# Performance work log

Measured on AMD Instinct MI355X. Metric: run time of the kernel, lower is better.

Reference implementation:

```python
import jax, jax.numpy as jnp
import numpy as np

N = 50000      # nodes
E = 800000     # edges (before self loops)
D_IN = 256     # input feature dim
H = 64         # hidden dim
HEADS = 4
NEG_SLOPE = 0.2  # PyG GATConv default


def setup_inputs() -> dict:
    key = jax.random.key(0)
    ks = jax.random.split(key, 24)

    def w(k, shape, fan_in):
        return jax.random.normal(k, shape, jnp.float32) / np.sqrt(fan_in)

    inp = {
        "x": jax.random.normal(ks[0], (N, D_IN), jnp.float32),
        "edge_index": jax.random.randint(ks[1], (2, E), 0, N, jnp.int64),
        # GCN layers
        "W0": w(ks[2], (D_IN, H), D_IN), "b0": jnp.zeros((H,), jnp.float32),
        "W1": w(ks[3], (H, H), H),       "b1": jnp.zeros((H,), jnp.float32),
        "W2": w(ks[4], (H, H), H),       "b2": jnp.zeros((H,), jnp.float32),
        # GAT
        "Wg": w(ks[5], (H, HEADS * H), H),
        "att_src": w(ks[6], (HEADS, H), H),
        "att_dst": w(ks[7], (HEADS, H), H),
        "bg": jnp.zeros((H,), jnp.float32),
        # classifier MLP: H -> H//2 -> 2
        "Wc1": w(ks[8], (H, H // 2), H),   "bc1": jnp.zeros((H // 2,), jnp.float32),
        "Wc2": w(ks[9], (H // 2, 2), H // 2), "bc2": jnp.zeros((2,), jnp.float32),
        # reconstructor MLP: H -> H -> D_IN
        "Wr1": w(ks[10], (H, H), H),       "br1": jnp.zeros((H,), jnp.float32),
        "Wr2": w(ks[11], (H, D_IN), H),    "br2": jnp.zeros((D_IN,), jnp.float32),
    }
    return inp


def reference(x, edge_index, W0, b0, W1, b1, W2, b2,
              Wg, att_src, att_dst, bg,
              Wc1, bc1, Wc2, bc2, Wr1, br1, Wr2, br2):
    # add self loops (PyG default for both GCNConv and GATConv)
    loops = jnp.arange(N, dtype=edge_index.dtype)
    src = jnp.concatenate([edge_index[0], loops])  # [E+N]
    dst = jnp.concatenate([edge_index[1], loops])

    # symmetric GCN normalization: deg^-1/2[src] * deg^-1/2[dst]
    deg = jax.ops.segment_sum(jnp.ones_like(src, jnp.float32), dst, num_segments=N)
    dinv = jnp.where(deg > 0, jax.lax.rsqrt(deg), 0.0)
    norm = dinv[src] * dinv[dst]  # [E+N]

    def gcn(h, W, b):
        msg = (h @ W)[src] * norm[:, None]          # gather + scale
        return jax.ops.segment_sum(msg, dst, num_segments=N) + b

    # stacked GCN with residuals (dropout inactive in eval)
    h = jax.nn.relu(gcn(x, W0, b0))                 # [N, H]
    h = h + jax.nn.relu(gcn(h, W1, b1))
    h = h + jax.nn.relu(gcn(h, W2, b2))

    # GAT layer, 4 heads, concat=False -> mean over heads
    xg = (h @ Wg).reshape(N, HEADS, H)              # [N, heads, H]
    a_s = jnp.einsum('nhf,hf->nh', xg, att_src)     # [N, heads]
    a_d = jnp.einsum('nhf,hf->nh', xg, att_dst)
    e = jax.nn.leaky_relu(a_s[src] + a_d[dst], NEG_SLOPE)  # [E+N, heads]
    m = jax.ops.segment_max(e, dst, num_segments=N)        # segment softmax
    ex = jnp.exp(e - m[dst])
    s = jax.ops.segment_sum(ex, dst, num_segments=N)
    alpha = ex / s[dst]                                     # [E+N, heads]
    hg = jax.ops.segment_sum(xg[src] * alpha[:, :, None], dst, num_segments=N)
    hg = hg.mean(axis=1) + bg                                # [N, H]

    # global mean pool (batch is None)
    h_global = hg.mean(axis=0, keepdims=True)                # [1, H]
    cls = jax.nn.relu(h_global @ Wc1 + bc1) @ Wc2 + bc2      # [1, 2]
    rec = jax.nn.relu(hg @ Wr1 + br1) @ Wr2 + br2            # [N, D_IN]
    return cls, rec, hg
```

## Files before the change

kernel.cpp:

```cpp
#include <hip/hip_runtime.h>

#define DIN 256
#define HD 64
#define NHEAD 4

static inline int cdiv(long a, long b) { return (int)((a + b - 1) / b); }

typedef __attribute__((ext_vector_type(8))) short bf16x8;
typedef __attribute__((ext_vector_type(4))) float f32x4;

__global__ __launch_bounds__(256) void k_filli(int* __restrict__ p, int v, int n) {
  int i = blockIdx.x * 256 + threadIdx.x;
  if (i < n) p[i] = v;
}

__global__ __launch_bounds__(256) void k_count(const int* __restrict__ dst,
                                               int* __restrict__ cnt, int E) {
  int i = blockIdx.x * 256 + threadIdx.x;
  if (i < E) atomicAdd(&cnt[dst[i]], 1);
}

__global__ __launch_bounds__(256) void k_bsum(const int* __restrict__ cnt,
                                              int* __restrict__ bsum, int n) {
  __shared__ int sd[256];
  int i = blockIdx.x * 256 + threadIdx.x;
  sd[threadIdx.x] = (i < n) ? cnt[i] : 0;
  __syncthreads();
  for (int o = 128; o > 0; o >>= 1) {
    if (threadIdx.x < o) sd[threadIdx.x] += sd[threadIdx.x + o];
    __syncthreads();
  }
  if (threadIdx.x == 0) bsum[blockIdx.x] = sd[0];
}

__global__ __launch_bounds__(256) void k_bscan(const int* __restrict__ bsum,
                                               int* __restrict__ boff, int B) {
  __shared__ int sd[256];
  int t = threadIdx.x;
  int v = (t < B) ? bsum[t] : 0;
  sd[t] = v;
  __syncthreads();
  for (int o = 1; o < 256; o <<= 1) {
    int x = (t >= o) ? sd[t - o] : 0;
    __syncthreads();
    sd[t] += x;
    __syncthreads();
  }
  if (t < B) boff[t] = sd[t] - v;
}

__global__ __launch_bounds__(256) void k_rowptr(const int* __restrict__ cnt,
                                                const int* __restrict__ boff,
                                                int* __restrict__ row_ptr,
                                                int* __restrict__ cursor,
                                                float* __restrict__ dinv,
                                                float* __restrict__ gsum, int n, int total) {
  __shared__ int sd[256];
  int t = threadIdx.x;
  int i = blockIdx.x * 256 + t;
  int v = (i < n) ? cnt[i] : 0;
  sd[t] = v;
  __syncthreads();
  for (int o = 1; o < 256; o <<= 1) {
    int x = (t >= o) ? sd[t - o] : 0;
    __syncthreads();
    sd[t] += x;
    __syncthreads();
  }
  if (i < n) {
    int rp = boff[blockIdx.x] + sd[t] - v;
    row_ptr[i] = rp;
    cursor[i] = rp;
    dinv[i] = rsqrtf((float)v);
  }
  if (i == n - 1) row_ptr[n] = total;
  if (blockIdx.x == 0 && t < 64) gsum[t] = 0.f;
}

__global__ __launch_bounds__(256) void k_csrfill(const int* __restrict__ src,
                                                 const int* __restrict__ dst,
                                                 int* __restrict__ cursor,
                                                 int* __restrict__ csr_src, int E, int n) {
  int e = blockIdx.x * 256 + threadIdx.x;
  if (e < E) {
    int pos = atomicAdd(&cursor[dst[e]], 1);
    csr_src[pos] = src[e];
  } else if (e < E + n) {
    int i = e - E;
    int pos = atomicAdd(&cursor[i], 1);
    csr_src[pos] = i;
  }
}

__device__ __forceinline__ unsigned short f2bf(float f) {
  unsigned u = __float_as_uint(f);
  u += 0x7FFFu + ((u >> 16) & 1u);
  return (unsigned short)(u >> 16);
}
__device__ __forceinline__ float bflo(unsigned u) { return __uint_as_float(u << 16); }
__device__ __forceinline__ float bfhi(unsigned u) { return __uint_as_float(u & 0xFFFF0000u); }

template <int KIN, int KOUT, int ATT>
__global__ __launch_bounds__(256, 4) void k_gmfma(const float* __restrict__ A,
                                                  const float* __restrict__ W,
                                                  unsigned short* __restrict__ c16, int n,
                                                  const float* __restrict__ attS,
                                                  const float* __restrict__ attD,
                                                  float* __restrict__ a_s,
                                                  float* __restrict__ a_d) {
  __shared__ unsigned short As[64][64];
  __shared__ unsigned short Wt[64][64];
  const int tid = threadIdx.x;
  const int m0 = blockIdx.x * 64;
  const int n0 = blockIdx.y * 64;
  const int lane = tid & 63;
  const int wid = tid >> 6;
  const int wm = wid * 16;
  const int fr = lane & 15;
  const int fg = lane >> 4;
  f32x4 acc[4] = {{0.f, 0.f, 0.f, 0.f},
                  {0.f, 0.f, 0.f, 0.f},
                  {0.f, 0.f, 0.f, 0.f},
                  {0.f, 0.f, 0.f, 0.f}};

  for (int k0 = 0; k0 < KIN; k0 += 64) {
    {
      int row = tid >> 3;
      int g = tid & 7;
#pragma unroll
      for (int q = 0; q < 2; ++q, row += 32) {
        int gr = m0 + row;
        gr = gr < n ? gr : n - 1;
        const float* ap = A + (size_t)gr * KIN + k0 + g * 8;
        float4 f0 = *(const float4*)ap;
        float4 f1 = *(const float4*)(ap + 4);
        uint4 pk;
        pk.x = (unsigned)f2bf(f0.x) | ((unsigned)f2bf(f0.y) << 16);
        pk.y = (unsigned)f2bf(f0.z) | ((unsigned)f2bf(f0.w) << 16);
        pk.z = (unsigned)f2bf(f1.x) | ((unsigned)f2bf(f1.y) << 16);
        pk.w = (unsigned)f2bf(f1.z) | ((unsigned)f2bf(f1.w) << 16);
        *(uint4*)&As[row][(g ^ (row & 7)) * 8] = pk;
      }
    }
    {
      int col = tid & 63;
      int kb = (tid >> 6) * 16;
      unsigned pk[8];
#pragma unroll
      for (int i = 0; i < 8; ++i) {
        float lo = W[(size_t)(k0 + kb + 2 * i) * KOUT + n0 + col];
        float hi = W[(size_t)(k0 + kb + 2 * i + 1) * KOUT + n0 + col];
        pk[i] = (unsigned)f2bf(lo) | ((unsigned)f2bf(hi) << 16);
      }
      int g0 = kb >> 3;
      uint4 w0; w0.x = pk[0]; w0.y = pk[1]; w0.z = pk[2]; w0.w = pk[3];
      uint4 w1; w1.x = pk[4]; w1.y = pk[5]; w1.z = pk[6]; w1.w = pk[7];
      *(uint4*)&Wt[col][((g0) ^ (col & 7)) * 8] = w0;
      *(uint4*)&Wt[col][((g0 + 1) ^ (col & 7)) * 8] = w1;
    }
    __syncthreads();
#pragma unroll
    for (int ks = 0; ks < 2; ++ks) {
      int ga = ks * 4 + fg;
      bf16x8 af = *(const bf16x8*)&As[wm + fr][(ga ^ (fr & 7)) * 8];
#pragma unroll
      for (int nt = 0; nt < 4; ++nt) {
        bf16x8 bfr = *(const bf16x8*)&Wt[nt * 16 + fr][(ga ^ (fr & 7)) * 8];
        acc[nt] = __builtin_amdgcn_mfma_f32_16x16x32_bf16(af, bfr, acc[nt], 0, 0, 0);
      }
    }
    __syncthreads();
  }

#pragma unroll
  for (int nt = 0; nt < 4; ++nt) {
#pragma unroll
    for (int r = 0; r < 4; ++r) {
      int row = m0 + wm + fg * 4 + r;
      if (row < n) {
        c16[(size_t)row * KOUT + n0 + nt * 16 + fr] = f2bf(acc[nt][r]);
      }
    }
  }
  if (ATT) {
    float attsv[4], attdv[4];
#pragma unroll
    for (int nt = 0; nt < 4; ++nt) {
      attsv[nt] = attS[n0 + nt * 16 + fr];
      attdv[nt] = attD[n0 + nt * 16 + fr];
    }
#pragma unroll
    for (int r = 0; r < 4; ++r) {
      float ps = acc[0][r] * attsv[0] + acc[1][r] * attsv[1] +
                 acc[2][r] * attsv[2] + acc[3][r] * attsv[3];
      float pd = acc[0][r] * attdv[0] + acc[1][r] * attdv[1] +
                 acc[2][r] * attdv[2] + acc[3][r] * attdv[3];
#pragma unroll
      for (int o = 1; o < 16; o <<= 1) {
        ps += __shfl_xor(ps, o);
        pd += __shfl_xor(pd, o);
      }
      int row = m0 + wm + fg * 4 + r;
      if (fr == 0 && row < n) {
        a_s[row * NHEAD + blockIdx.y] = ps;
        a_d[row * NHEAD + blockIdx.y] = pd;
      }
    }
  }
}

template <int KIN, int KOUT, int MODE>
__global__ __launch_bounds__(256, 4) void k_gemm2(const float* __restrict__ A,
                                                  const float* __restrict__ W,
                                                  const float* __restrict__ bias,
                                                  float* __restrict__ C, int n) {
  constexpr int LD = 68;
  __shared__ float As[64][LD];
  __shared__ float Ws[64][LD];
  const int tid = threadIdx.x;
  const int tx = tid & 15;
  const int ty = tid >> 4;
  const int m0 = blockIdx.x * 64;
  const int n0 = blockIdx.y * 64;
  const int lr = tid >> 4;
  const int lc = (tid & 15) * 4;
  float acc[4][4] = {};

  for (int k0 = 0; k0 < KIN; k0 += 64) {
#pragma unroll
    for (int q = 0; q < 4; ++q) {
      int r = lr + q * 16;
      int gr = m0 + r;
      gr = gr < n ? gr : n - 1;
      *(float4*)&As[r][lc] = *(const float4*)(A + (size_t)gr * KIN + k0 + lc);
      *(float4*)&Ws[r][lc] = *(const float4*)(W + (size_t)(k0 + r) * KOUT + n0 + lc);
    }
    __syncthreads();
#pragma unroll 2
    for (int k = 0; k < 64; k += 4) {
      float4 a0 = *(const float4*)&As[ty][k];
      float4 a1 = *(const float4*)&As[ty + 16][k];
      float4 a2 = *(const float4*)&As[ty + 32][k];
      float4 a3 = *(const float4*)&As[ty + 48][k];
      float4 w0 = *(const float4*)&Ws[k + 0][tx * 4];
      float4 w1 = *(const float4*)&Ws[k + 1][tx * 4];
      float4 w2 = *(const float4*)&Ws[k + 2][tx * 4];
      float4 w3 = *(const float4*)&Ws[k + 3][tx * 4];
#define FMA_ROW(i, av)                                                   \
      acc[i][0] = fmaf(av.x, w0.x, fmaf(av.y, w1.x, fmaf(av.z, w2.x, fmaf(av.w, w3.x, acc[i][0])))); \
      acc[i][1] = fmaf(av.x, w0.y, fmaf(av.y, w1.y, fmaf(av.z, w2.y, fmaf(av.w, w3.y, acc[i][1])))); \
      acc[i][2] = fmaf(av.x, w0.z, fmaf(av.y, w1.z, fmaf(av.z, w2.z, fmaf(av.w, w3.z, acc[i][2])))); \
      acc[i][3] = fmaf(av.x, w0.w, fmaf(av.y, w1.w, fmaf(av.z, w2.w, fmaf(av.w, w3.w, acc[i][3]))));
      FMA_ROW(0, a0)
      FMA_ROW(1, a1)
      FMA_ROW(2, a2)
      FMA_ROW(3, a3)
#undef FMA_ROW
    }
    __syncthreads();
  }

  float4 bv = *(const float4*)(bias + n0 + tx * 4);
#pragma unroll
  for (int i = 0; i < 4; ++i) {
    int gr = m0 + ty + 16 * i;
    float4 r;
    r.x = acc[i][0] + bv.x; r.y = acc[i][1] + bv.y;
    r.z = acc[i][2] + bv.z; r.w = acc[i][3] + bv.w;
    if (MODE == 1) {
      r.x = r.x > 0.f ? r.x : 0.f; r.y = r.y > 0.f ? r.y : 0.f;
      r.z = r.z > 0.f ? r.z : 0.f; r.w = r.w > 0.f ? r.w : 0.f;
    }
    if (gr < n) {
      if (MODE == 2) {
        float2 lo; lo.x = r.x; lo.y = r.y;
        float2 hi; hi.x = r.z; hi.y = r.w;
        *(float2*)(C + (size_t)gr * KOUT + n0 + tx * 4) = lo;
        *(float2*)(C + (size_t)gr * KOUT + n0 + tx * 4 + 2) = hi;
      } else {
        *(float4*)(C + (size_t)gr * KOUT + n0 + tx * 4) = r;
      }
    }
  }
}

__global__ __launch_bounds__(256) void k_agg16(const unsigned short* __restrict__ P16,
                                               const int* __restrict__ csr_src,
                                               const int* __restrict__ row_ptr,
                                               const float* __restrict__ dinv,
                                               const float* __restrict__ bias,
                                               const float* __restrict__ resid,
                                               float* __restrict__ out, int n) {
  int node = (blockIdx.x * 256 + threadIdx.x) >> 6;
  int lane = threadIdx.x & 63;
  if (node >= n) return;
  int beg = row_ptr[node], end = row_ptr[node + 1];
  int q = lane & 15, qw = lane >> 4;
  float a0 = 0.f, a1 = 0.f, a2 = 0.f, a3 = 0.f;
  for (int i = beg + qw; i < end; i += 4) {
    int s = csr_src[i];
    float d = dinv[s];
    uint2 v = *(const uint2*)(P16 + (size_t)s * HD + q * 4);
    a0 = fmaf(bflo(v.x), d, a0);
    a1 = fmaf(bfhi(v.x), d, a1);
    a2 = fmaf(bflo(v.y), d, a2);
    a3 = fmaf(bfhi(v.y), d, a3);
  }
  a0 += __shfl_xor(a0, 16); a1 += __shfl_xor(a1, 16);
  a2 += __shfl_xor(a2, 16); a3 += __shfl_xor(a3, 16);
  a0 += __shfl_xor(a0, 32); a1 += __shfl_xor(a1, 32);
  a2 += __shfl_xor(a2, 32); a3 += __shfl_xor(a3, 32);
  if (lane < 16) {
    float dn = dinv[node];
    float4 bv = *(const float4*)(bias + q * 4);
    float4 o;
    o.x = a0 * dn + bv.x; o.y = a1 * dn + bv.y;
    o.z = a2 * dn + bv.z; o.w = a3 * dn + bv.w;
    o.x = o.x > 0.f ? o.x : 0.f; o.y = o.y > 0.f ? o.y : 0.f;
    o.z = o.z > 0.f ? o.z : 0.f; o.w = o.w > 0.f ? o.w : 0.f;
    if (resid) {
      float4 rr = *(const float4*)(resid + (size_t)node * HD + q * 4);
      o.x += rr.x; o.y += rr.y; o.z += rr.z; o.w += rr.w;
    }
    *(float4*)(out + (size_t)node * HD + q * 4) = o;
  }
}

__device__ __forceinline__ float leaky(float v) { return v > 0.f ? v : 0.2f * v; }

__global__ __launch_bounds__(256) void k_gat(const unsigned short* __restrict__ xg16,
                                             const float* __restrict__ a_s,
                                             const float* __restrict__ a_d,
                                             const int* __restrict__ csr_src,
                                             const int* __restrict__ row_ptr,
                                             float* __restrict__ galpha,
                                             const float* __restrict__ bg,
                                             float* __restrict__ hg,
                                             float* __restrict__ hga,
                                             int n) {
  __shared__ float4 ew[4][128];
  const int wid = threadIdx.x >> 6;
  const int node = (blockIdx.x * 256 + threadIdx.x) >> 6;
  const int lane = threadIdx.x & 63;
  if (node >= n) return;
  const int beg = row_ptr[node], end = row_ptr[node + 1];
  const bool uselds = (end - beg) <= 128;
  float4 ad = ((const float4*)a_d)[node];

  float m0 = -1e30f, m1 = -1e30f, m2 = -1e30f, m3 = -1e30f;
  float4 e0, e1;
  const int i0 = beg + lane, i1 = beg + lane + 64;
  if (uselds) {
    if (i0 < end) {
      int s = csr_src[i0];
      float4 as = ((const float4*)a_s)[s];
      e0.x = leaky(as.x + ad.x); e0.y = leaky(as.y + ad.y);
      e0.z = leaky(as.z + ad.z); e0.w = leaky(as.w + ad.w);
      m0 = e0.x; m1 = e0.y; m2 = e0.z; m3 = e0.w;
    }
    if (i1 < end) {
      int s = csr_src[i1];
      float4 as = ((const float4*)a_s)[s];
      e1.x = leaky(as.x + ad.x); e1.y = leaky(as.y + ad.y);
      e1.z = leaky(as.z + ad.z); e1.w = leaky(as.w + ad.w);
      m0 = fmaxf(m0, e1.x); m1 = fmaxf(m1, e1.y);
      m2 = fmaxf(m2, e1.z); m3 = fmaxf(m3, e1.w);
    }
  } else {
    for (int i = i0; i < end; i += 64) {
      int s = csr_src[i];
      float4 as = ((const float4*)a_s)[s];
      float4 e;
      e.x = leaky(as.x + ad.x); e.y = leaky(as.y + ad.y);
      e.z = leaky(as.z + ad.z); e.w = leaky(as.w + ad.w);
      ((float4*)galpha)[i] = e;
      m0 = fmaxf(m0, e.x); m1 = fmaxf(m1, e.y);
      m2 = fmaxf(m2, e.z); m3 = fmaxf(m3, e.w);
    }
    __threadfence();
  }
#pragma unroll
  for (int o = 32; o > 0; o >>= 1) {
    m0 = fmaxf(m0, __shfl_xor(m0, o));
    m1 = fmaxf(m1, __shfl_xor(m1, o));
    m2 = fmaxf(m2, __shfl_xor(m2, o));
    m3 = fmaxf(m3, __shfl_xor(m3, o));
  }

  float s0 = 0.f, s1 = 0.f, s2 = 0.f, s3 = 0.f;
  if (uselds) {
    if (i0 < end) {
      float4 ex;
      ex.x = expf(e0.x - m0); ex.y = expf(e0.y - m1);
      ex.z = expf(e0.z - m2); ex.w = expf(e0.w - m3);
      ew[wid][i0 - beg] = ex;
      s0 += ex.x; s1 += ex.y; s2 += ex.z; s3 += ex.w;
    }
    if (i1 < end) {
      float4 ex;
      ex.x = expf(e1.x - m0); ex.y = expf(e1.y - m1);
      ex.z = expf(e1.z - m2); ex.w = expf(e1.w - m3);
      ew[wid][i1 - beg] = ex;
      s0 += ex.x; s1 += ex.y; s2 += ex.z; s3 += ex.w;
    }
  } else {
    for (int i = i0; i < end; i += 64) {
      float4 e = ((const float4*)galpha)[i];
      float4 ex;
      ex.x = expf(e.x - m0); ex.y = expf(e.y - m1);
      ex.z = expf(e.z - m2); ex.w = expf(e.w - m3);
      ((float4*)galpha)[i] = ex;
      s0 += ex.x; s1 += ex.y; s2 += ex.z; s3 += ex.w;
    }
    __threadfence();
  }
#pragma unroll
  for (int o = 32; o > 0; o >>= 1) {
    s0 += __shfl_xor(s0, o);
    s1 += __shfl_xor(s1, o);
    s2 += __shfl_xor(s2, o);
    s3 += __shfl_xor(s3, o);
  }
  float r0 = 0.25f / s0, r1 = 0.25f / s1, r2 = 0.25f / s2, r3 = 0.25f / s3;

  const int head = lane >> 4;
  const int fo = (lane & 15) * 4;
  float rh = head == 0 ? r0 : head == 1 ? r1 : head == 2 ? r2 : r3;
  float aA0 = 0.f, aA1 = 0.f, aA2 = 0.f, aA3 = 0.f;
  float aB0 = 0.f, aB1 = 0.f, aB2 = 0.f, aB3 = 0.f;
  float aC0 = 0.f, aC1 = 0.f, aC2 = 0.f, aC3 = 0.f;
  float aD0 = 0.f, aD1 = 0.f, aD2 = 0.f, aD3 = 0.f;

#define P3_BODY(ALPHA_AT)                                                        \
  {                                                                              \
    int i = beg;                                                                 \
    for (; i + 4 <= end; i += 4) {                                               \
      int sA = csr_src[i], sB = csr_src[i + 1];                                  \
      int sC = csr_src[i + 2], sD = csr_src[i + 3];                              \
      float alA = ALPHA_AT(i), alB = ALPHA_AT(i + 1);                            \
      float alC = ALPHA_AT(i + 2), alD = ALPHA_AT(i + 3);                        \
      uint2 vA = *(const uint2*)(xg16 + (size_t)sA * 256 + lane * 4);            \
      uint2 vB = *(const uint2*)(xg16 + (size_t)sB * 256 + lane * 4);            \
      uint2 vC = *(const uint2*)(xg16 + (size_t)sC * 256 + lane * 4);            \
      uint2 vD = *(const uint2*)(xg16 + (size_t)sD * 256 + lane * 4);            \
      aA0 = fmaf(bflo(vA.x), alA, aA0); aA1 = fmaf(bfhi(vA.x), alA, aA1);        \
      aA2 = fmaf(bflo(vA.y), alA, aA2); aA3 = fmaf(bfhi(vA.y), alA, aA3);        \
      aB0 = fmaf(bflo(vB.x), alB, aB0); aB1 = fmaf(bfhi(vB.x), alB, aB1);        \
      aB2 = fmaf(bflo(vB.y), alB, aB2); aB3 = fmaf(bfhi(vB.y), alB, aB3);        \
      aC0 = fmaf(bflo(vC.x), alC, aC0); aC1 = fmaf(bfhi(vC.x), alC, aC1);        \
      aC2 = fmaf(bflo(vC.y), alC, aC2); aC3 = fmaf(bfhi(vC.y), alC, aC3);        \
      aD0 = fmaf(bflo(vD.x), alD, aD0); aD1 = fmaf(bfhi(vD.x), alD, aD1);        \
      aD2 = fmaf(bflo(vD.y), alD, aD2); aD3 = fmaf(bfhi(vD.y), alD, aD3);        \
    }                                                                            \
    for (; i < end; ++i) {                                                       \
      int s = csr_src[i];                                                        \
      float al = ALPHA_AT(i);                                                    \
      uint2 v = *(const uint2*)(xg16 + (size_t)s * 256 + lane * 4);              \
      aA0 = fmaf(bflo(v.x), al, aA0); aA1 = fmaf(bfhi(v.x), al, aA1);            \
      aA2 = fmaf(bflo(v.y), al, aA2); aA3 = fmaf(bfhi(v.y), al, aA3);            \
    }                                                                            \
  }

  if (uselds) {
    const float* ap = (const float*)&ew[wid][0];
#define AL_LDS(idx) ap[((idx) - beg) * 4 + head]
    P3_BODY(AL_LDS)
#undef AL_LDS
  } else {
#define AL_GBL(idx) galpha[(size_t)(idx) * 4 + head]
    P3_BODY(AL_GBL)
#undef AL_GBL
  }
#undef P3_BODY

  float t0 = (aA0 + aB0 + aC0 + aD0) * rh;
  float t1 = (aA1 + aB1 + aC1 + aD1) * rh;
  float t2 = (aA2 + aB2 + aC2 + aD2) * rh;
  float t3 = (aA3 + aB3 + aC3 + aD3) * rh;
  t0 += __shfl_xor(t0, 16); t1 += __shfl_xor(t1, 16);
  t2 += __shfl_xor(t2, 16); t3 += __shfl_xor(t3, 16);
  t0 += __shfl_xor(t0, 32); t1 += __shfl_xor(t1, 32);
  t2 += __shfl_xor(t2, 32); t3 += __shfl_xor(t3, 32);
  if (lane < 16) {
    float4 o;
    o.x = t0 + bg[fo]; o.y = t1 + bg[fo + 1];
    o.z = t2 + bg[fo + 2]; o.w = t3 + bg[fo + 3];
    *(float4*)(hga + (size_t)node * HD + fo) = o;
    float2 lo; lo.x = o.x; lo.y = o.y;
    float2 hi; hi.x = o.z; hi.y = o.w;
    *(float2*)(hg + (size_t)node * HD + fo) = lo;
    *(float2*)(hg + (size_t)node * HD + fo + 2) = hi;
  }
}

__global__ __launch_bounds__(256) void k_gsum(const float* __restrict__ hg,
                                              float* __restrict__ gsum, int n) {
  __shared__ float red[256];
  int f = threadIdx.x & 63, g = threadIdx.x >> 6;
  float local = 0.f;
  for (int nd = blockIdx.x * 4 + g; nd < n; nd += gridDim.x * 4)
    local += hg[(size_t)nd * HD + f];
  red[threadIdx.x] = local;
  __syncthreads();
  if (threadIdx.x < 64)
    atomicAdd(&gsum[f], red[f] + red[64 + f] + red[128 + f] + red[192 + f]);
}

__global__ __launch_bounds__(64) void k_cls(const float* __restrict__ gsum,
                                            const float* __restrict__ Wc1,
                                            const float* __restrict__ bc1,
                                            const float* __restrict__ Wc2,
                                            const float* __restrict__ bc2,
                                            float* __restrict__ out, int n) {
  __shared__ float hgl[64];
  __shared__ float t1[32];
  int t = threadIdx.x;
  hgl[t] = gsum[t] / (float)n;
  __syncthreads();
  if (t < 32) {
    float a = bc1[t];
#pragma unroll 16
    for (int f = 0; f < 64; ++f) a = fmaf(hgl[f], Wc1[f * 32 + t], a);
    t1[t] = a > 0.f ? a : 0.f;
  }
  __syncthreads();
  if (t < 2) {
    float a = bc2[t];
#pragma unroll
    for (int j = 0; j < 32; ++j) a = fmaf(t1[j], Wc2[j * 2 + t], a);
    out[t] = a;
  }
}

extern "C" void kernel_launch(void* const* d_in, const int* in_sizes, int n_in,
                              void* d_out, int out_size, void* d_ws, size_t ws_size,
                              hipStream_t stream) {
  const float* x = (const float*)d_in[0];
  const int* ei = (const int*)d_in[1];
  const float* W0 = (const float*)d_in[2];
  const float* b0 = (const float*)d_in[3];
  const float* W1 = (const float*)d_in[4];
  const float* b1 = (const float*)d_in[5];
  const float* W2 = (const float*)d_in[6];
  const float* b2 = (const float*)d_in[7];
  const float* Wg = (const float*)d_in[8];
  const float* att_src = (const float*)d_in[9];
  const float* att_dst = (const float*)d_in[10];
  const float* bg = (const float*)d_in[11];
  const float* Wc1 = (const float*)d_in[12];
  const float* bc1 = (const float*)d_in[13];
  const float* Wc2 = (const float*)d_in[14];
  const float* bc2 = (const float*)d_in[15];
  const float* Wr1 = (const float*)d_in[16];
  const float* br1 = (const float*)d_in[17];
  const float* Wr2 = (const float*)d_in[18];
  const float* br2 = (const float*)d_in[19];

  const int n = in_sizes[0] / DIN;
  const int E = in_sizes[1] / 2;
  const int nE = E + n;
  const int* src = ei;
  const int* dst = ei + E;

  float* ws = (float*)d_ws;
  size_t off = 0;
  auto alloc = [&](size_t nelems) {
    float* p = ws + off;
    off += (nelems + 63) & ~(size_t)63;
    return p;
  };
  int* CNT = (int*)alloc(n);
  int* BSUM = (int*)alloc(256);
  int* BOFF = (int*)alloc(256);
  int* ROWP = (int*)alloc(n + 1);
  int* CURS = (int*)alloc(n);
  int* CSRS = (int*)alloc(nE);
  float* DINV = alloc(n);
  float* P = alloc((size_t)n * 256);
  unsigned short* XG16 = (unsigned short*)alloc((size_t)n * 128);
  unsigned short* P16 = (unsigned short*)alloc((size_t)n * 32);
  float* Hb = alloc((size_t)n * HD);
  float* HG = alloc((size_t)n * HD);
  float* ASD = alloc((size_t)n * NHEAD);
  float* ADD = alloc((size_t)n * NHEAD);
  float* GALPHA = alloc((size_t)nE * NHEAD);
  float* GSUM = alloc(64);
  (void)ws_size;

  float* out = (float*)d_out;
  float* out_cls = out;
  float* out_rec = out + 2;
  float* out_hg = out + 2 + (size_t)n * 256;

  const int TB = 256;
  const int B = cdiv(n, TB);
  const int GM = cdiv(n, 64);

  k_filli<<<cdiv(n, TB), TB, 0, stream>>>(CNT, 1, n);
  k_count<<<cdiv(E, TB), TB, 0, stream>>>(dst, CNT, E);
  k_bsum<<<B, TB, 0, stream>>>(CNT, BSUM, n);
  k_bscan<<<1, TB, 0, stream>>>(BSUM, BOFF, B);
  k_rowptr<<<B, TB, 0, stream>>>(CNT, BOFF, ROWP, CURS, DINV, GSUM, n, nE);
  k_csrfill<<<cdiv(nE, TB), TB, 0, stream>>>(src, dst, CURS, CSRS, E, n);

  k_gmfma<256, 64, 0><<<dim3(GM, 1), TB, 0, stream>>>(x, W0, P16, n,
                                                      nullptr, nullptr, nullptr, nullptr);
  k_agg16<<<cdiv((long)n * 64, TB), TB, 0, stream>>>(P16, CSRS, ROWP, DINV, b0, nullptr, Hb, n);

  k_gmfma<64, 64, 0><<<dim3(GM, 1), TB, 0, stream>>>(Hb, W1, P16, n,
                                                     nullptr, nullptr, nullptr, nullptr);
  k_agg16<<<cdiv((long)n * 64, TB), TB, 0, stream>>>(P16, CSRS, ROWP, DINV, b1, Hb, Hb, n);

  k_gmfma<64, 64, 0><<<dim3(GM, 1), TB, 0, stream>>>(Hb, W2, P16, n,
                                                     nullptr, nullptr, nullptr, nullptr);
  k_agg16<<<cdiv((long)n * 64, TB), TB, 0, stream>>>(P16, CSRS, ROWP, DINV, b2, Hb, Hb, n);

  k_gmfma<64, 256, 1><<<dim3(GM, 4), TB, 0, stream>>>(Hb, Wg, XG16, n,
                                                      att_src, att_dst, ASD, ADD);
  k_gat<<<cdiv((long)n * 64, TB), TB, 0, stream>>>(XG16, ASD, ADD, CSRS, ROWP, GALPHA, bg,
                                                   out_hg, HG, n);

  k_gsum<<<512, TB, 0, stream>>>(HG, GSUM, n);
  k_cls<<<1, 64, 0, stream>>>(GSUM, Wc1, bc1, Wc2, bc2, out_cls, n);
  k_gemm2<64, 64, 1><<<dim3(GM, 1), TB, 0, stream>>>(HG, Wr1, br1, P, n);
  k_gemm2<64, 256, 2><<<dim3(GM, 4), TB, 0, stream>>>(P, Wr2, br2, out_rec, n);
}
```

Before: 381.0 us.

## Use MFMA GEMM for reconstructor MLP and widen gather loads in aggregation

Replaces the fp32 FMA reconstructor GEMMs with the bf16 MFMA kernel, which gains a bias/ReLU fp32 epilogue. The GCN aggregation is restructured so each lane loads 16 bytes (8 bf16 features) and 8 edges are processed in parallel per wavefront. The GAT aggregation uses the same wider per-lane loads, with two interleaved accumulator sets over half-wave edge streams. Together these aim to cut FMA-bound GEMM time and raise memory-level parallelism in the gathers, at the cost of bf16 rounding in the reconstructor matmuls and more shuffle reductions.

```diff
diff --git a/kernel.cpp b/kernel.cpp
--- a/kernel.cpp
+++ b/kernel.cpp
@@ -100,14 +100,16 @@
 __device__ __forceinline__ float bflo(unsigned u) { return __uint_as_float(u << 16); }
 __device__ __forceinline__ float bfhi(unsigned u) { return __uint_as_float(u & 0xFFFF0000u); }
 
-template <int KIN, int KOUT, int ATT>
+template <int KIN, int KOUT, int ATT, int EPI>
 __global__ __launch_bounds__(256, 4) void k_gmfma(const float* __restrict__ A,
                                                   const float* __restrict__ W,
                                                   unsigned short* __restrict__ c16, int n,
                                                   const float* __restrict__ attS,
                                                   const float* __restrict__ attD,
                                                   float* __restrict__ a_s,
-                                                  float* __restrict__ a_d) {
+                                                  float* __restrict__ a_d,
+                                                  const float* __restrict__ bias,
+                                                  float* __restrict__ Cf) {
   __shared__ unsigned short As[64][64];
   __shared__ unsigned short Wt[64][64];
   const int tid = threadIdx.x;
@@ -172,13 +174,27 @@
     __syncthreads();
   }
 
-#pragma unroll
-  for (int nt = 0; nt < 4; ++nt) {
-#pragma unroll
-    for (int r = 0; r < 4; ++r) {
-      int row = m0 + wm + fg * 4 + r;
-      if (row < n) {
-        c16[(size_t)row * KOUT + n0 + nt * 16 + fr] = f2bf(acc[nt][r]);
+  if (EPI == 0) {
+#pragma unroll
+    for (int nt = 0; nt < 4; ++nt) {
+#pragma unroll
+      for (int r = 0; r < 4; ++r) {
+        int row = m0 + wm + fg * 4 + r;
+        if (row < n) c16[(size_t)row * KOUT + n0 + nt * 16 + fr] = f2bf(acc[nt][r]);
+      }
+    }
+  } else {
+    float bv[4];
+#pragma unroll
+    for (int nt = 0; nt < 4; ++nt) bv[nt] = bias[n0 + nt * 16 + fr];
+#pragma unroll
+    for (int nt = 0; nt < 4; ++nt) {
+#pragma unroll
+      for (int r = 0; r < 4; ++r) {
+        int row = m0 + wm + fg * 4 + r;
+        float v = acc[nt][r] + bv[nt];
+        if (EPI == 1) v = v > 0.f ? v : 0.f;
+        if (row < n) Cf[(size_t)row * KOUT + n0 + nt * 16 + fr] = v;
       }
     }
   }
@@ -204,81 +220,6 @@
       if (fr == 0 && row < n) {
         a_s[row * NHEAD + blockIdx.y] = ps;
         a_d[row * NHEAD + blockIdx.y] = pd;
-      }
-    }
-  }
-}
-
-template <int KIN, int KOUT, int MODE>
-__global__ __launch_bounds__(256, 4) void k_gemm2(const float* __restrict__ A,
-                                                  const float* __restrict__ W,
-                                                  const float* __restrict__ bias,
-                                                  float* __restrict__ C, int n) {
-  constexpr int LD = 68;
-  __shared__ float As[64][LD];
-  __shared__ float Ws[64][LD];
-  const int tid = threadIdx.x;
-  const int tx = tid & 15;
-  const int ty = tid >> 4;
-  const int m0 = blockIdx.x * 64;
-  const int n0 = blockIdx.y * 64;
-  const int lr = tid >> 4;
-  const int lc = (tid & 15) * 4;
-  float acc[4][4] = {};
-
-  for (int k0 = 0; k0 < KIN; k0 += 64) {
-#pragma unroll
-    for (int q = 0; q < 4; ++q) {
-      int r = lr + q * 16;
-      int gr = m0 + r;
-      gr = gr < n ? gr : n - 1;
-      *(float4*)&As[r][lc] = *(const float4*)(A + (size_t)gr * KIN + k0 + lc);
-      *(float4*)&Ws[r][lc] = *(const float4*)(W + (size_t)(k0 + r) * KOUT + n0 + lc);
-    }
-    __syncthreads();
-#pragma unroll 2
-    for (int k = 0; k < 64; k += 4) {
-      float4 a0 = *(const float4*)&As[ty][k];
-      float4 a1 = *(const float4*)&As[ty + 16][k];
-      float4 a2 = *(const float4*)&As[ty + 32][k];
-      float4 a3 = *(const float4*)&As[ty + 48][k];
-      float4 w0 = *(const float4*)&Ws[k + 0][tx * 4];
-      float4 w1 = *(const float4*)&Ws[k + 1][tx * 4];
-      float4 w2 = *(const float4*)&Ws[k + 2][tx * 4];
-      float4 w3 = *(const float4*)&Ws[k + 3][tx * 4];
-#define FMA_ROW(i, av)                                                   \
-      acc[i][0] = fmaf(av.x, w0.x, fmaf(av.y, w1.x, fmaf(av.z, w2.x, fmaf(av.w, w3.x, acc[i][0])))); \
-      acc[i][1] = fmaf(av.x, w0.y, fmaf(av.y, w1.y, fmaf(av.z, w2.y, fmaf(av.w, w3.y, acc[i][1])))); \
-      acc[i][2] = fmaf(av.x, w0.z, fmaf(av.y, w1.z, fmaf(av.z, w2.z, fmaf(av.w, w3.z, acc[i][2])))); \
-      acc[i][3] = fmaf(av.x, w0.w, fmaf(av.y, w1.w, fmaf(av.z, w2.w, fmaf(av.w, w3.w, acc[i][3]))));
-      FMA_ROW(0, a0)
-      FMA_ROW(1, a1)
-      FMA_ROW(2, a2)
-      FMA_ROW(3, a3)
-#undef FMA_ROW
-    }
-    __syncthreads();
-  }
-
-  float4 bv = *(const float4*)(bias + n0 + tx * 4);
-#pragma unroll
-  for (int i = 0; i < 4; ++i) {
-    int gr = m0 + ty + 16 * i;
-    float4 r;
-    r.x = acc[i][0] + bv.x; r.y = acc[i][1] + bv.y;
-    r.z = acc[i][2] + bv.z; r.w = acc[i][3] + bv.w;
-    if (MODE == 1) {
-      r.x = r.x > 0.f ? r.x : 0.f; r.y = r.y > 0.f ? r.y : 0.f;
-      r.z = r.z > 0.f ? r.z : 0.f; r.w = r.w > 0.f ? r.w : 0.f;
-    }
-    if (gr < n) {
-      if (MODE == 2) {
-        float2 lo; lo.x = r.x; lo.y = r.y;
-        float2 hi; hi.x = r.z; hi.y = r.w;
-        *(float2*)(C + (size_t)gr * KOUT + n0 + tx * 4) = lo;
-        *(float2*)(C + (size_t)gr * KOUT + n0 + tx * 4 + 2) = hi;
-      } else {
-        *(float4*)(C + (size_t)gr * KOUT + n0 + tx * 4) = r;
       }
     }
   }
@@ -295,34 +236,44 @@
   int lane = threadIdx.x & 63;
   if (node >= n) return;
   int beg = row_ptr[node], end = row_ptr[node + 1];
-  int q = lane & 15, qw = lane >> 4;
-  float a0 = 0.f, a1 = 0.f, a2 = 0.f, a3 = 0.f;
-  for (int i = beg + qw; i < end; i += 4) {
+  int es = lane >> 3;
+  int fo = (lane & 7) * 8;
+  float a[8] = {};
+  for (int i = beg + es; i < end; i += 8) {
     int s = csr_src[i];
     float d = dinv[s];
-    uint2 v = *(const uint2*)(P16 + (size_t)s * HD + q * 4);
-    a0 = fmaf(bflo(v.x), d, a0);
-    a1 = fmaf(bfhi(v.x), d, a1);
-    a2 = fmaf(bflo(v.y), d, a2);
-    a3 = fmaf(bfhi(v.y), d, a3);
-  }
-  a0 += __shfl_xor(a0, 16); a1 += __shfl_xor(a1, 16);
-  a2 += __shfl_xor(a2, 16); a3 += __shfl_xor(a3, 16);
-  a0 += __shfl_xor(a0, 32); a1 += __shfl_xor(a1, 32);
-  a2 += __shfl_xor(a2, 32); a3 += __shfl_xor(a3, 32);
-  if (lane < 16) {
+    uint4 v = *(const uint4*)(P16 + (size_t)s * HD + fo);
+    a[0] = fmaf(bflo(v.x), d, a[0]); a[1] = fmaf(bfhi(v.x), d, a[1]);
+    a[2] = fmaf(bflo(v.y), d, a[2]); a[3] = fmaf(bfhi(v.y), d, a[3]);
+    a[4] = fmaf(bflo(v.z), d, a[4]); a[5] = fmaf(bfhi(v.z), d, a[5]);
+    a[6] = fmaf(bflo(v.w), d, a[6]); a[7] = fmaf(bfhi(v.w), d, a[7]);
+  }
+#pragma unroll
+  for (int o = 8; o < 64; o <<= 1) {
+#pragma unroll
+    for (int k = 0; k < 8; ++k) a[k] += __shfl_xor(a[k], o);
+  }
+  if (lane < 8) {
     float dn = dinv[node];
-    float4 bv = *(const float4*)(bias + q * 4);
-    float4 o;
-    o.x = a0 * dn + bv.x; o.y = a1 * dn + bv.y;
-    o.z = a2 * dn + bv.z; o.w = a3 * dn + bv.w;
-    o.x = o.x > 0.f ? o.x : 0.f; o.y = o.y > 0.f ? o.y : 0.f;
-    o.z = o.z > 0.f ? o.z : 0.f; o.w = o.w > 0.f ? o.w : 0.f;
+    float4 b0 = *(const float4*)(bias + fo);
+    float4 b1 = *(const float4*)(bias + fo + 4);
+    float o0[8];
+    o0[0] = a[0] * dn + b0.x; o0[1] = a[1] * dn + b0.y;
+    o0[2] = a[2] * dn + b0.z; o0[3] = a[3] * dn + b0.w;
+    o0[4] = a[4] * dn + b1.x; o0[5] = a[5] * dn + b1.y;
+    o0[6] = a[6] * dn + b1.z; o0[7] = a[7] * dn + b1.w;
+#pragma unroll
+    for (int k = 0; k < 8; ++k) o0[k] = o0[k] > 0.f ? o0[k] : 0.f;
     if (resid) {
-      float4 rr = *(const float4*)(resid + (size_t)node * HD + q * 4);
-      o.x += rr.x; o.y += rr.y; o.z += rr.z; o.w += rr.w;
-    }
-    *(float4*)(out + (size_t)node * HD + q * 4) = o;
+      float4 r0 = *(const float4*)(resid + (size_t)node * HD + fo);
+      float4 r1 = *(const float4*)(resid + (size_t)node * HD + fo + 4);
+      o0[0] += r0.x; o0[1] += r0.y; o0[2] += r0.z; o0[3] += r0.w;
+      o0[4] += r1.x; o0[5] += r1.y; o0[6] += r1.z; o0[7] += r1.w;
+    }
+    float4 w0; w0.x = o0[0]; w0.y = o0[1]; w0.z = o0[2]; w0.w = o0[3];
+    float4 w1; w1.x = o0[4]; w1.y = o0[5]; w1.z = o0[6]; w1.w = o0[7];
+    *(float4*)(out + (size_t)node * HD + fo) = w0;
+    *(float4*)(out + (size_t)node * HD + fo + 4) = w1;
   }
 }
 
@@ -423,42 +374,34 @@
   }
   float r0 = 0.25f / s0, r1 = 0.25f / s1, r2 = 0.25f / s2, r3 = 0.25f / s3;
 
-  const int head = lane >> 4;
-  const int fo = (lane & 15) * 4;
-  float rh = head == 0 ? r0 : head == 1 ? r1 : head == 2 ? r2 : r3;
-  float aA0 = 0.f, aA1 = 0.f, aA2 = 0.f, aA3 = 0.f;
-  float aB0 = 0.f, aB1 = 0.f, aB2 = 0.f, aB3 = 0.f;
-  float aC0 = 0.f, aC1 = 0.f, aC2 = 0.f, aC3 = 0.f;
-  float aD0 = 0.f, aD1 = 0.f, aD2 = 0.f, aD3 = 0.f;
-
-#define P3_BODY(ALPHA_AT)                                                        \
-  {                                                                              \
-    int i = beg;                                                                 \
-    for (; i + 4 <= end; i += 4) {                                               \
-      int sA = csr_src[i], sB = csr_src[i + 1];                                  \
-      int sC = csr_src[i + 2], sD = csr_src[i + 3];                              \
-      float alA = ALPHA_AT(i), alB = ALPHA_AT(i + 1);                            \
-      float alC = ALPHA_AT(i + 2), alD = ALPHA_AT(i + 3);                        \
-      uint2 vA = *(const uint2*)(xg16 + (size_t)sA * 256 + lane * 4);            \
-      uint2 vB = *(const uint2*)(xg16 + (size_t)sB * 256 + lane * 4);            \
-      uint2 vC = *(const uint2*)(xg16 + (size_t)sC * 256 + lane * 4);            \
-      uint2 vD = *(const uint2*)(xg16 + (size_t)sD * 256 + lane * 4);            \
-      aA0 = fmaf(bflo(vA.x), alA, aA0); aA1 = fmaf(bfhi(vA.x), alA, aA1);        \
-      aA2 = fmaf(bflo(vA.y), alA, aA2); aA3 = fmaf(bfhi(vA.y), alA, aA3);        \
-      aB0 = fmaf(bflo(vB.x), alB, aB0); aB1 = fmaf(bfhi(vB.x), alB, aB1);        \
-      aB2 = fmaf(bflo(vB.y), alB, aB2); aB3 = fmaf(bfhi(vB.y), alB, aB3);        \
-      aC0 = fmaf(bflo(vC.x), alC, aC0); aC1 = fmaf(bfhi(vC.x), alC, aC1);        \
-      aC2 = fmaf(bflo(vC.y), alC, aC2); aC3 = fmaf(bfhi(vC.y), alC, aC3);        \
-      aD0 = fmaf(bflo(vD.x), alD, aD0); aD1 = fmaf(bfhi(vD.x), alD, aD1);        \
-      aD2 = fmaf(bflo(vD.y), alD, aD2); aD3 = fmaf(bfhi(vD.y), alD, aD3);        \
-    }                                                                            \
-    for (; i < end; ++i) {                                                       \
-      int s = csr_src[i];                                                        \
-      float al = ALPHA_AT(i);                                                    \
-      uint2 v = *(const uint2*)(xg16 + (size_t)s * 256 + lane * 4);              \
-      aA0 = fmaf(bflo(v.x), al, aA0); aA1 = fmaf(bfhi(v.x), al, aA1);            \
-      aA2 = fmaf(bflo(v.y), al, aA2); aA3 = fmaf(bfhi(v.y), al, aA3);            \
-    }                                                                            \
+  const int hl = lane & 31;
+  const int hw = lane >> 5;
+  const int head = hl >> 3;
+  float a[8] = {}, b[8] = {};
+
+#define GATHER8(ACC, S, AL)                                                     \
+  {                                                                             \
+    uint4 v = *(const uint4*)(xg16 + (size_t)(S) * 256 + hl * 8);               \
+    ACC[0] = fmaf(bflo(v.x), AL, ACC[0]); ACC[1] = fmaf(bfhi(v.x), AL, ACC[1]); \
+    ACC[2] = fmaf(bflo(v.y), AL, ACC[2]); ACC[3] = fmaf(bfhi(v.y), AL, ACC[3]); \
+    ACC[4] = fmaf(bflo(v.z), AL, ACC[4]); ACC[5] = fmaf(bfhi(v.z), AL, ACC[5]); \
+    ACC[6] = fmaf(bflo(v.w), AL, ACC[6]); ACC[7] = fmaf(bfhi(v.w), AL, ACC[7]); \
+  }
+
+#define P3_BODY(ALPHA_AT)                                  \
+  {                                                        \
+    int i = beg + hw;                                      \
+    for (; i + 2 < end; i += 4) {                          \
+      int sA = csr_src[i], sB = csr_src[i + 2];            \
+      float alA = ALPHA_AT(i), alB = ALPHA_AT(i + 2);      \
+      GATHER8(a, sA, alA)                                  \
+      GATHER8(b, sB, alB)                                  \
+    }                                                      \
+    for (; i < end; i += 2) {                              \
+      int s = csr_src[i];                                  \
+      float al = ALPHA_AT(i);                              \
+      GATHER8(a, s, al)                                    \
+    }                                                      \
   }
 
   if (uselds) {
@@ -472,24 +415,35 @@
 #undef AL_GBL
   }
 #undef P3_BODY
-
-  float t0 = (aA0 + aB0 + aC0 + aD0) * rh;
-  float t1 = (aA1 + aB1 + aC1 + aD1) * rh;
-  float t2 = (aA2 + aB2 + aC2 + aD2) * rh;
-  float t3 = (aA3 + aB3 + aC3 + aD3) * rh;
-  t0 += __shfl_xor(t0, 16); t1 += __shfl_xor(t1, 16);
-  t2 += __shfl_xor(t2, 16); t3 += __shfl_xor(t3, 16);
-  t0 += __shfl_xor(t0, 32); t1 += __shfl_xor(t1, 32);
-  t2 += __shfl_xor(t2, 32); t3 += __shfl_xor(t3, 32);
-  if (lane < 16) {
-    float4 o;
-    o.x = t0 + bg[fo]; o.y = t1 + bg[fo + 1];
-    o.z = t2 + bg[fo + 2]; o.w = t3 + bg[fo + 3];
-    *(float4*)(hga + (size_t)node * HD + fo) = o;
-    float2 lo; lo.x = o.x; lo.y = o.y;
-    float2 hi; hi.x = o.z; hi.y = o.w;
-    *(float2*)(hg + (size_t)node * HD + fo) = lo;
-    *(float2*)(hg + (size_t)node * HD + fo + 2) = hi;
+#undef GATHER8
+
+  float rh = head == 0 ? r0 : head == 1 ? r1 : head == 2 ? r2 : r3;
+  float t[8];
+#pragma unroll
+  for (int k = 0; k < 8; ++k) {
+    t[k] = a[k] + b[k];
+    t[k] += __shfl_xor(t[k], 32);
+    t[k] *= rh;
+    t[k] += __shfl_xor(t[k], 8);
+    t[k] += __shfl_xor(t[k], 16);
+  }
+  if (lane < 8) {
+    int f0 = lane * 8;
+    float o0[8];
+#pragma unroll
+    for (int k = 0; k < 8; ++k) o0[k] = t[k] + bg[f0 + k];
+    float4 w0; w0.x = o0[0]; w0.y = o0[1]; w0.z = o0[2]; w0.w = o0[3];
+    float4 w1; w1.x = o0[4]; w1.y = o0[5]; w1.z = o0[6]; w1.w = o0[7];
+    *(float4*)(hga + (size_t)node * HD + f0) = w0;
+    *(float4*)(hga + (size_t)node * HD + f0 + 4) = w1;
+    float2 p0; p0.x = o0[0]; p0.y = o0[1];
+    float2 p1; p1.x = o0[2]; p1.y = o0[3];
+    float2 p2; p2.x = o0[4]; p2.y = o0[5];
+    float2 p3; p3.x = o0[6]; p3.y = o0[7];
+    *(float2*)(hg + (size_t)node * HD + f0) = p0;
+    *(float2*)(hg + (size_t)node * HD + f0 + 2) = p1;
+    *(float2*)(hg + (size_t)node * HD + f0 + 4) = p2;
+    *(float2*)(hg + (size_t)node * HD + f0 + 6) = p3;
   }
 }
 
@@ -603,25 +557,27 @@
   k_rowptr<<<B, TB, 0, stream>>>(CNT, BOFF, ROWP, CURS, DINV, GSUM, n, nE);
   k_csrfill<<<cdiv(nE, TB), TB, 0, stream>>>(src, dst, CURS, CSRS, E, n);
 
-  k_gmfma<256, 64, 0><<<dim3(GM, 1), TB, 0, stream>>>(x, W0, P16, n,
-                                                      nullptr, nullptr, nullptr, nullptr);
+  k_gmfma<256, 64, 0, 0><<<dim3(GM, 1), TB, 0, stream>>>(
+      x, W0, P16, n, nullptr, nullptr, nullptr, nullptr, nullptr, nullptr);
   k_agg16<<<cdiv((long)n * 64, TB), TB, 0, stream>>>(P16, CSRS, ROWP, DINV, b0, nullptr, Hb, n);
 
-  k_gmfma<64, 64, 0><<<dim3(GM, 1), TB, 0, stream>>>(Hb, W1, P16, n,
-                                                     nullptr, nullptr, nullptr, nullptr);
+  k_gmfma<64, 64, 0, 0><<<dim3(GM, 1), TB, 0, stream>>>(
+      Hb, W1, P16, n, nullptr, nullptr, nullptr, nullptr, nullptr, nullptr);
   k_agg16<<<cdiv((long)n * 64, TB), TB, 0, stream>>>(P16, CSRS, ROWP, DINV, b1, Hb, Hb, n);
 
-  k_gmfma<64, 64, 0><<<dim3(GM, 1), TB, 0, stream>>>(Hb, W2, P16, n,
-                                                     nullptr, nullptr, nullptr, nullptr);
+  k_gmfma<64, 64, 0, 0><<<dim3(GM, 1), TB, 0, stream>>>(
+      Hb, W2, P16, n, nullptr, nullptr, nullptr, nullptr, nullptr, nullptr);
   k_agg16<<<cdiv((long)n * 64, TB), TB, 0, stream>>>(P16, CSRS, ROWP, DINV, b2, Hb, Hb, n);
 
-  k_gmfma<64, 256, 1><<<dim3(GM, 4), TB, 0, stream>>>(Hb, Wg, XG16, n,
-                                                      att_src, att_dst, ASD, ADD);
+  k_gmfma<64, 256, 1, 0><<<dim3(GM, 4), TB, 0, stream>>>(
+      Hb, Wg, XG16, n, att_src, att_dst, ASD, ADD, nullptr, nullptr);
   k_gat<<<cdiv((long)n * 64, TB), TB, 0, stream>>>(XG16, ASD, ADD, CSRS, ROWP, GALPHA, bg,
                                                    out_hg, HG, n);
 
   k_gsum<<<512, TB, 0, stream>>>(HG, GSUM, n);
   k_cls<<<1, 64, 0, stream>>>(GSUM, Wc1, bc1, Wc2, bc2, out_cls, n);
-  k_gemm2<64, 64, 1><<<dim3(GM, 1), TB, 0, stream>>>(HG, Wr1, br1, P, n);
-  k_gemm2<64, 256, 2><<<dim3(GM, 4), TB, 0, stream>>>(P, Wr2, br2, out_rec, n);
-}
+  k_gmfma<64, 64, 0, 1><<<dim3(GM, 1), TB, 0, stream>>>(
+      HG, Wr1, nullptr, n, nullptr, nullptr, nullptr, nullptr, br1, P);
+  k_gmfma<64, 256, 0, 2><<<dim3(GM, 4), TB, 0, stream>>>(
+      P, Wr2, nullptr, n, nullptr, nullptr, nullptr, nullptr, br2, out_rec);
+}
```

After: 352.0 us. -7.6%, faster.
